# Kernel optimization log

Measured on AMD Instinct MI355X. Metric: run time of the kernel, lower is better.

The kernel has to match this reference:

```python
import jax, jax.numpy as jnp
import numpy as np

BINS = 32
NUM_ACTION = 12


def _conv(x, w, b, stride, pad):
    y = jax.lax.conv_general_dilated(x, w, (stride, stride), [(pad, pad), (pad, pad)],
                                     dimension_numbers=('NCHW', 'OIHW', 'NCHW'))
    return y + b[None, :, None, None]


def _maxpool3s2(x):
    return jax.lax.reduce_window(x, -jnp.inf, jax.lax.max, (1, 1, 3, 3), (1, 1, 2, 2), 'VALID')


def _area_resize(x, oh, ow):
    b, c, h, w = x.shape  # exact area interp when h%oh==0, w%ow==0
    return x.reshape(b, c, oh, h // oh, ow, w // ow).mean(axis=(3, 5))


def _sobel_mag(gray):
    # kornia.filters.Sobel: normalized sobel kernels (abs-sum=1), replicate pad, sqrt(gx^2+gy^2+eps)
    kx = jnp.array([[-1., 0., 1.], [-2., 0., 2.], [-1., 0., 1.]], jnp.float32) / 8.0
    k = jnp.stack([kx, kx.T])[:, None]  # [2,1,3,3]
    p = jnp.pad(gray, ((0, 0), (0, 0), (1, 1), (1, 1)), mode='edge')
    g = jax.lax.conv_general_dilated(p, k, (1, 1), 'VALID',
                                     dimension_numbers=('NCHW', 'OIHW', 'NCHW'))
    return jnp.sqrt(jnp.sum(g * g, axis=1, keepdims=True) + 1e-6)


def _hist_feature(img):
    # Fused replacement for FeatureExtractor's python triple-loop of torch.histc calls.
    # img: [B,1,H,W] with values in [0,1]. Scale 0: whole-image hist; scale 1: the 4
    # quadrants of the full-res image; third bins-slot stays zero (loop only runs 2 scales).
    b, _, h, w = img.shape
    idx = jnp.clip((img[:, 0] * BINS).astype(jnp.int32), 0, BINS - 1)  # [B,H,W]
    hist = lambda i: jnp.zeros((BINS,), jnp.float32).at[i.ravel()].add(1.0)
    h0 = jax.vmap(hist)(idx) / (h * w)                                  # [B,BINS]
    h2, w2 = h // 2, w // 2
    blocks = idx.reshape(b, 2, h2, 2, w2).transpose(0, 1, 3, 2, 4).reshape(b * 4, h2 * w2)
    h1 = jax.vmap(hist)(blocks).reshape(b, 2, 2, BINS) / (h2 * w2)      # [B,2,2,BINS]
    out0 = jnp.broadcast_to(h0[:, :, None, None], (b, BINS, 4, 4))
    out1 = jnp.repeat(jnp.repeat(h1.transpose(0, 3, 1, 2), 2, axis=2), 2, axis=3)
    out2 = jnp.zeros_like(out0)
    return jnp.concatenate([out0, out1, out2], axis=1)                  # [B,3*BINS,4,4]


def _l2norm(x):
    return x / (jnp.linalg.norm(x, axis=1, keepdims=True) + 1e-7)


def _forward(image, w1, b1, w2, b2, w3, b3, w4, b4, w5, b5, fc1_w, fc1_b, fc2_w, fc2_b):
    b = image.shape[0]
    rgb = jnp.stack([image[:, 0], 0.5 * (image[:, 1] + image[:, 2]), image[:, 3]], axis=1)
    # AlexNet conv backbone on area-resized 112x112 -> [B,256,2,2]
    x = _area_resize(rgb, 112, 112)
    x = _maxpool3s2(jax.nn.relu(_conv(x, w1, b1, 4, 2)))
    x = _maxpool3s2(jax.nn.relu(_conv(x, w2, b2, 1, 2)))
    x = jax.nn.relu(_conv(x, w3, b3, 1, 1))
    x = jax.nn.relu(_conv(x, w4, b4, 1, 1))
    x = _maxpool3s2(jax.nn.relu(_conv(x, w5, b5, 1, 1)))
    f_sem = x.reshape(b, -1)                                            # [B,1024]
    gray = (0.299 * rgb[:, 0] + 0.587 * rgb[:, 1] + 0.114 * rgb[:, 2])[:, None]
    f_inten = _hist_feature(gray).reshape(b, -1)                        # [B,1536]
    f_grad = _hist_feature(_sobel_mag(gray)).reshape(b, -1)             # [B,1536]
    f_cat = jnp.concatenate([_l2norm(f_sem), _l2norm(f_inten), _l2norm(f_grad)], axis=1)
    h = jax.nn.relu(f_cat)                                              # Dropout = identity (eval)
    h = jax.nn.relu(h @ fc1_w.T + fc1_b)
    return h @ fc2_w.T + fc2_b                                          # [B,NUM_ACTION]


def setup_inputs() -> dict:
    key = jax.random.key(0)
    ks = jax.random.split(key, 8)
    B = 64
    image = jax.random.uniform(ks[0], (B, 4, 448, 448), jnp.float32)
    w = lambda k, shape, s=0.02: jax.random.normal(k, shape, jnp.float32) * s
    return {
        'image': image,
        'w1': w(ks[1], (64, 3, 11, 11)), 'b1': jnp.zeros((64,), jnp.float32),
        'w2': w(ks[2], (192, 64, 5, 5)), 'b2': jnp.zeros((192,), jnp.float32),
        'w3': w(ks[3], (384, 192, 3, 3)), 'b3': jnp.zeros((384,), jnp.float32),
        'w4': w(ks[4], (256, 384, 3, 3)), 'b4': jnp.zeros((256,), jnp.float32),
        'w5': w(ks[5], (256, 256, 3, 3)), 'b5': jnp.zeros((256,), jnp.float32),
        'fc1_w': w(ks[6], (256, 4096), 0.01), 'fc1_b': jnp.zeros((256,), jnp.float32),
        'fc2_w': w(ks[7], (NUM_ACTION, 256), 0.05), 'fc2_b': jnp.zeros((NUM_ACTION,), jnp.float32),
    }


def reference(image, w1, b1, w2, b2, w3, b3, w4, b4, w5, b5, fc1_w, fc1_b, fc2_w, fc2_b):
    return _forward(image, w1, b1, w2, b2, w3, b3, w4, b4, w5, b5, fc1_w, fc1_b, fc2_w, fc2_b)
```

## Files before the change

### kernel.cpp

```cpp
#include <hip/hip_runtime.h>
#include <math.h>

typedef __attribute__((ext_vector_type(8))) short short8;
typedef __attribute__((ext_vector_type(8))) unsigned short u16x8;
typedef __attribute__((ext_vector_type(4))) float f32x4;
typedef unsigned short ushort_t;

constexpr size_t OFF_HINT = 0;
constexpr size_t OFF_HGRD = OFF_HINT + (size_t)64*160;
constexpr size_t OFF_F    = OFF_HGRD + (size_t)64*160;
constexpr size_t OFF_H1   = OFF_F    + (size_t)64*4096;
constexpr size_t OFF_P5   = OFF_H1   + (size_t)64*256;
constexpr size_t OFF_WHI  = OFF_P5   + (size_t)64*1024;
constexpr size_t W1_OFF = 0;         constexpr int K1T = 363,  K1R = 384;
constexpr size_t W2_OFF = 24576;     constexpr int K2T = 1600, K2R = 1664;
constexpr size_t W3_OFF = 344064;    constexpr int K3T = 1728, K3R = 1792;
constexpr size_t W4_OFF = 1032192;   constexpr int K4T = 3456, K4R = 3456;
constexpr size_t W5_OFF = 1916928;   constexpr int K5T = 2304, K5R = 2304;
constexpr size_t WP_U16 = 2506752;
constexpr size_t OFF_WLO  = OFF_WHI + WP_U16/2;
constexpr size_t OFF_RA   = OFF_WLO + WP_U16/2;
constexpr size_t SZ_RA    = (size_t)2583552/2;
constexpr size_t A4P_U16  = 786432;
constexpr size_t OFF_RB   = OFF_RA + SZ_RA;
constexpr size_t SZ_RB    = (size_t)2985984/2;
constexpr size_t WS_FLOATS = OFF_RB + SZ_RB;

__device__ __forceinline__ void bf16split(float v, unsigned short& hi, unsigned short& lo) {
  union { float f; unsigned u; } a; a.f = v;
  unsigned uh = (a.u + 0x7FFFu + ((a.u >> 16) & 1u)) >> 16;
  hi = (unsigned short)uh;
  union { unsigned u; float f; } b; b.u = uh << 16;
  float rem = v - b.f;
  union { float f; unsigned u; } c; c.f = rem;
  lo = (unsigned short)((c.u + 0x7FFFu + ((c.u >> 16) & 1u)) >> 16);
}
__device__ __forceinline__ ushort_t f2bf(float f) {
  union { float f; unsigned u; } a; a.f = f;
  return (ushort_t)((a.u + 0x7FFFu + ((a.u >> 16) & 1u)) >> 16);
}
__device__ __forceinline__ float bf2f(ushort_t u) {
  union { unsigned u; float f; } a; a.u = ((unsigned)u) << 16; return a.f;
}

__global__ __launch_bounds__(256) void k_wsplit_all(const float* __restrict__ w1,
                                                    const float* __restrict__ w2,
                                                    const float* __restrict__ w3,
                                                    const float* __restrict__ w4,
                                                    const float* __restrict__ w5,
                                                    ushort_t* __restrict__ whi,
                                                    ushort_t* __restrict__ wlo) {
  const size_t idx = (size_t)blockIdx.x * 256 + threadIdx.x;
  if (idx >= WP_U16) return;
  const float* w; int kt, kr; size_t base;
  if (idx < W2_OFF)                { w = w1; kt = K1T; kr = K1R; base = W1_OFF; }
  else if (idx < W3_OFF)           { w = w2; kt = K2T; kr = K2R; base = W2_OFF; }
  else if (idx < W4_OFF)           { w = w3; kt = K3T; kr = K3R; base = W3_OFF; }
  else if (idx < W5_OFF)           { w = w4; kt = K4T; kr = K4R; base = W4_OFF; }
  else                             { w = w5; kt = K5T; kr = K5R; base = W5_OFF; }
  const size_t rel = idx - base;
  const int m = (int)(rel / kr), k = (int)(rel - (size_t)m * kr);
  const float v = (k < kt) ? w[(size_t)m * kt + k] : 0.f;
  unsigned short h, l;
  bf16split(v, h, l);
  whi[idx] = h; wlo[idx] = l;
}

__global__ __launch_bounds__(256) void k_preproc(const float* __restrict__ img,
                                                 float* __restrict__ hint,
                                                 float* __restrict__ hgrd,
                                                 ushort_t* __restrict__ x0) {
  const int b = blockIdx.x, s = blockIdx.y;
  const int r0 = s * 8;
  __shared__ float gs[10][448];
  __shared__ unsigned char lh[64 * 260];
  __shared__ ushort_t part[8 * 112 * 3];
  const int tid = threadIdx.x;
  for (int i = tid; i < (64 * 260) / 4; i += 256) ((unsigned*)lh)[i] = 0u;
  const float* ib = img + (size_t)b * 4 * 200704;
  for (int i = tid; i < 10 * 112; i += 256) {
    const int rr = i / 112, cc = i % 112, c4 = cc * 4;
    int r = r0 + rr - 1; r = r < 0 ? 0 : (r > 447 ? 447 : r);
    const size_t o = (size_t)r * 448 + c4;
    const float4 vr = *(const float4*)&ib[o];
    const float4 g1 = *(const float4*)&ib[200704 + o];
    const float4 g2 = *(const float4*)&ib[2 * 200704 + o];
    const float4 vb = *(const float4*)&ib[3 * 200704 + o];
    float4 g;
    g.x = 0.299f * vr.x + 0.587f * (0.5f * (g1.x + g2.x)) + 0.114f * vb.x;
    g.y = 0.299f * vr.y + 0.587f * (0.5f * (g1.y + g2.y)) + 0.114f * vb.y;
    g.z = 0.299f * vr.z + 0.587f * (0.5f * (g1.z + g2.z)) + 0.114f * vb.z;
    g.w = 0.299f * vr.w + 0.587f * (0.5f * (g1.w + g2.w)) + 0.114f * vb.w;
    *(float4*)&gs[rr][c4] = g;
    if (rr >= 1 && rr <= 8) {
      const float sr = vr.x + vr.y + vr.z + vr.w;
      const float sg = 0.5f * (g1.x + g2.x) + 0.5f * (g1.y + g2.y)
                     + 0.5f * (g1.z + g2.z) + 0.5f * (g1.w + g2.w);
      const float sb = vb.x + vb.y + vb.z + vb.w;
      ushort_t* pp = &part[((rr - 1) * 112 + cc) * 3];
      pp[0] = f2bf(sr); pp[1] = f2bf(sg); pp[2] = f2bf(sb);
    }
  }
  __syncthreads();
  for (int i = tid; i < 672; i += 256) {
    const int cc = i % 112;
    const int t  = i / 112;
    const int or2 = t & 1, ch = t >> 1;
    float sum = 0.f;
    #pragma unroll
    for (int rw = 0; rw < 4; ++rw)
      sum += bf2f(part[((or2 * 4 + rw) * 112 + cc) * 3 + ch]);
    x0[(((size_t)b * 3 + ch) * 116 + 2 + 2 * s + or2) * 116 + 2 + cc] = f2bf(sum * (1.f / 16.f));
  }
  for (int i = tid; i < 8 * 112; i += 256) {
    const int dr = i / 112, c4 = (i % 112) * 4;
    const unsigned colbit = (c4 >= 224) ? 1u : 0u;
    const float4 m1 = *(const float4*)&gs[dr + 1][c4];
    const float gv[4] = {m1.x, m1.y, m1.z, m1.w};
    #pragma unroll
    for (int j = 0; j < 4; ++j) {
      int bin = (int)(gv[j] * 32.f); bin = bin > 31 ? 31 : (bin < 0 ? 0 : bin);
      lh[(colbit * 32u + (unsigned)bin) * 260u + (unsigned)tid]++;
    }
  }
  __syncthreads();
  const unsigned rowbit = (s >= 28) ? 1u : 0u;
  {
    const int key = tid >> 2, quarter = tid & 3;
    const unsigned* row = (const unsigned*)&lh[(unsigned)key * 260u];
    unsigned sum = 0;
    #pragma unroll
    for (int d = 0; d < 16; ++d) {
      const unsigned v = row[quarter * 16 + d];
      sum += (v & 0xFFu) + ((v >> 8) & 0xFFu) + ((v >> 16) & 0xFFu) + (v >> 24);
    }
    sum += __shfl_down(sum, 1, 64);
    sum += __shfl_down(sum, 2, 64);
    if (quarter == 0) {
      const int colbit2 = key >> 5, bin = key & 31;
      atomicAdd(&hint[(size_t)b * 160 + 32 + (rowbit * 2 + colbit2) * 32 + bin], (float)sum);
    }
  }
  __syncthreads();
  for (int i = tid; i < (64 * 260) / 4; i += 256) ((unsigned*)lh)[i] = 0u;
  __syncthreads();
  for (int i = tid; i < 8 * 112; i += 256) {
    const int dr = i / 112, c4 = (i % 112) * 4;
    const unsigned colbit = (c4 >= 224) ? 1u : 0u;
    const int cl = c4 > 0 ? c4 - 1 : 0;
    const int cr = c4 < 444 ? c4 + 4 : 447;
    const float4 m0 = *(const float4*)&gs[dr][c4];
    const float4 m1 = *(const float4*)&gs[dr + 1][c4];
    const float4 m2 = *(const float4*)&gs[dr + 2][c4];
    const float r0v[6] = {gs[dr][cl],     m0.x, m0.y, m0.z, m0.w, gs[dr][cr]};
    const float r1v[6] = {gs[dr + 1][cl], m1.x, m1.y, m1.z, m1.w, gs[dr + 1][cr]};
    const float r2v[6] = {gs[dr + 2][cl], m2.x, m2.y, m2.z, m2.w, gs[dr + 2][cr]};
    #pragma unroll
    for (int j = 0; j < 4; ++j) {
      const float gx = (-r0v[j] + r0v[j + 2] - 2.f * r1v[j] + 2.f * r1v[j + 2]
                        - r2v[j] + r2v[j + 2]) * 0.125f;
      const float gy = (-r0v[j] - 2.f * r0v[j + 1] - r0v[j + 2]
                        + r2v[j] + 2.f * r2v[j + 1] + r2v[j + 2]) * 0.125f;
      const float mag = sqrtf(gx * gx + gy * gy + 1e-6f);
      int sb = (int)(mag * 32.f); sb = sb > 31 ? 31 : (sb < 0 ? 0 : sb);
      lh[(colbit * 32u + (unsigned)sb) * 260u + (unsigned)tid]++;
    }
  }
  __syncthreads();
  {
    const int key = tid >> 2, quarter = tid & 3;
    const unsigned* row = (const unsigned*)&lh[(unsigned)key * 260u];
    unsigned sum = 0;
    #pragma unroll
    for (int d = 0; d < 16; ++d) {
      const unsigned v = row[quarter * 16 + d];
      sum += (v & 0xFFu) + ((v >> 8) & 0xFFu) + ((v >> 16) & 0xFFu) + (v >> 24);
    }
    sum += __shfl_down(sum, 1, 64);
    sum += __shfl_down(sum, 2, 64);
    if (quarter == 0) {
      const int colbit2 = key >> 5, bin = key & 31;
      atomicAdd(&hgrd[(size_t)b * 160 + 32 + (rowbit * 2 + colbit2) * 32 + bin], (float)sum);
    }
  }
}

template<int CIN, int HP, int WP, int KH, int KW, int STRIDE, int OH, int OW,
         int OHP, int OWP, int OPAD, int M, int MT>
__global__ __launch_bounds__(512) void k_conv_mfma(const ushort_t* __restrict__ in,
                                                   const ushort_t* __restrict__ whi_,
                                                   const ushort_t* __restrict__ wlo_,
                                                   const float* __restrict__ bias,
                                                   ushort_t* __restrict__ out) {
  constexpr int K_TOT  = CIN * KH * KW;
  constexpr int K_ROUND = ((K_TOT + 127) / 128) * 128;
  constexpr int GSTEPS = K_ROUND / 128;
  constexpr int KHW = KH * KW;
  constexpr int NPB = OH * OW;
  constexpr int WROWS = MT / 16;
  constexpr int TGRP  = 4 / WROWS;
  constexpr int TFRAG = 4 / TGRP;
  __shared__ ushort_t Bs[2][2][64 * 64];
  __shared__ ushort_t ftab[K_ROUND];
  const int tid = threadIdx.x;
  const int lane = tid & 63, wv = tid >> 6;
  const int g = wv >> 2, wg = wv & 3;
  const int sub = tid & 255;
  const int n0 = blockIdx.x * 64, m0 = blockIdx.y * MT;
  for (int k = tid; k < K_ROUND; k += 512) {
    const int c = k / KHW, kr = k - c * KHW;
    const int ky = kr / KW, kx = kr - (kr / KW) * KW;
    ftab[k] = (k < K_TOT) ? (ushort_t)(2 * ((c * HP + ky) * WP + kx)) : (ushort_t)0;
  }
  const int col = sub & 63, kc2 = sub >> 6;
  const int nb = n0 + col;
  const int bB = nb / NPB, rB = nb % NPB;
  const int oyB = rB / OW, oxB = rB % OW;
  const char* baseB = (const char*)(in + (size_t)bB * CIN * HP * WP)
                      + 2 * (oyB * STRIDE * WP + oxB * STRIDE);
  const int wm = wg % WROWS, tg = wg / WROWS;
  const int mrow = m0 + wm * 16 + (lane & 15);
  const ushort_t* wh = whi_ + (size_t)mrow * K_ROUND;
  const ushort_t* wl = wlo_ + (size_t)mrow * K_ROUND;
  const int kA = (lane >> 4) * 8;
  f32x4 acc[TFRAG] = {};
  const int kb0 = g * GSTEPS * 64;
  __syncthreads();

  u16x8 rb0, rb1;
  short8 rah0, ral0, rah1, ral1;
  {
    const int kb = kb0;
    const u16x8 f0 = *(const u16x8*)&ftab[kb + kc2 * 16];
    const u16x8 f1 = *(const u16x8*)&ftab[kb + kc2 * 16 + 8];
    #pragma unroll
    for (int j = 0; j < 8; ++j) rb0[j] = *(const ushort_t*)(baseB + f0[j]);
    #pragma unroll
    for (int j = 0; j < 8; ++j) rb1[j] = *(const ushort_t*)(baseB + f1[j]);
    rah0 = *(const short8*)&wh[kb + kA];
    ral0 = *(const short8*)&wl[kb + kA];
    rah1 = *(const short8*)&wh[kb + 32 + kA];
    ral1 = *(const short8*)&wl[kb + 32 + kA];
  }
  {
    const int c0 = kc2 * 2, c1 = c0 + 1;
    *(u16x8*)&Bs[g][0][col * 64 + ((c0 ^ (col & 7)) * 8)] = rb0;
    *(u16x8*)&Bs[g][0][col * 64 + ((c1 ^ (col & 7)) * 8)] = rb1;
  }
  __syncthreads();
  int cur = 0;
  for (int step = 0; step < GSTEPS; ++step) {
    const short8 a_h0 = rah0, a_l0 = ral0, a_h1 = rah1, a_l1 = ral1;
    if (step + 1 < GSTEPS) {
      const int kb = kb0 + (step + 1) * 64;
      const u16x8 f0 = *(const u16x8*)&ftab[kb + kc2 * 16];
      const u16x8 f1 = *(const u16x8*)&ftab[kb + kc2 * 16 + 8];
      #pragma unroll
      for (int j = 0; j < 8; ++j) rb0[j] = *(const ushort_t*)(baseB + f0[j]);
      #pragma unroll
      for (int j = 0; j < 8; ++j) rb1[j] = *(const ushort_t*)(baseB + f1[j]);
      rah0 = *(const short8*)&wh[kb + kA];
      ral0 = *(const short8*)&wl[kb + kA];
      rah1 = *(const short8*)&wh[kb + 32 + kA];
      ral1 = *(const short8*)&wl[kb + 32 + kA];
    }
    #pragma unroll
    for (int s = 0; s < 2; ++s) {
      const short8 a_h = s ? a_h1 : a_h0;
      const short8 a_l = s ? a_l1 : a_l0;
      const int cA = s * 4 + (lane >> 4);
      #pragma unroll
      for (int tt = 0; tt < TFRAG; ++tt) {
        const int t = tg * TFRAG + tt;
        const int coln = t * 16 + (lane & 15);
        const short8 b_v = *(const short8*)&Bs[g][cur][coln * 64 + ((cA ^ (coln & 7)) * 8)];
        acc[tt] = __builtin_amdgcn_mfma_f32_16x16x32_bf16(a_h, b_v, acc[tt], 0, 0, 0);
        acc[tt] = __builtin_amdgcn_mfma_f32_16x16x32_bf16(a_l, b_v, acc[tt], 0, 0, 0);
      }
    }
    if (step + 1 < GSTEPS) {
      const int c0 = kc2 * 2, c1 = c0 + 1;
      *(u16x8*)&Bs[g][cur ^ 1][col * 64 + ((c0 ^ (col & 7)) * 8)] = rb0;
      *(u16x8*)&Bs[g][cur ^ 1][col * 64 + ((c1 ^ (col & 7)) * 8)] = rb1;
      __syncthreads();
      cur ^= 1;
    }
  }
  __syncthreads();
  float* scratch = (float*)&Bs[0][0][0];
  if (g == 1) {
    #pragma unroll
    for (int tt = 0; tt < TFRAG; ++tt) {
      const int t = tg * TFRAG + tt;
      #pragma unroll
      for (int q = 0; q < 4; ++q)
        scratch[(wm * 16 + (lane >> 4) * 4 + q) * 64 + t * 16 + (lane & 15)] = acc[tt][q];
    }
  }
  __syncthreads();
  if (g == 0) {
    #pragma unroll
    for (int q = 0; q < 4; ++q) {
      const int m = m0 + wm * 16 + (lane >> 4) * 4 + q;
      const float bi = bias[m];
      #pragma unroll
      for (int tt = 0; tt < TFRAG; ++tt) {
        const int t = tg * TFRAG + tt;
        const int n = n0 + t * 16 + (lane & 15);
        const float v = acc[tt][q]
                      + scratch[(wm * 16 + (lane >> 4) * 4 + q) * 64 + t * 16 + (lane & 15)]
                      + bi;
        const int b = n / NPB, r = n % NPB;
        const int oy = r / OW, ox = r - (r / OW) * OW;
        out[(((size_t)b * M + m) * OHP + OPAD + oy) * OWP + OPAD + ox] = f2bf(fmaxf(v, 0.f));
      }
    }
  }
}

template<int C, int HI, int HO, int HOP, int PAD, bool OUTF32>
__global__ __launch_bounds__(256) void k_pool(const ushort_t* __restrict__ in,
                                              void* __restrict__ out) {
  const int idx = blockIdx.x * 256 + threadIdx.x;
  constexpr int TOT = 64 * C * HOP * HOP;
  if (idx >= TOT) return;
  const int x = idx % HOP;
  const int y = (idx / HOP) % HOP;
  const int c = (idx / (HOP * HOP)) % C;
  const int b = idx / (HOP * HOP * C);
  ushort_t v = 0;
  const int oy = y - PAD, ox = x - PAD;
  if (oy >= 0 && oy < HO && ox >= 0 && ox < HO) {
    const ushort_t* ib = in + (size_t)(b * C + c) * HI * HI + (size_t)(oy * 2) * HI + ox * 2;
    #pragma unroll
    for (int i = 0; i < 3; ++i)
      #pragma unroll
      for (int j = 0; j < 3; ++j) {
        const ushort_t u = ib[i * HI + j];
        v = u > v ? u : v;
      }
  }
  if constexpr (OUTF32) ((float*)out)[idx] = bf2f(v);
  else                  ((ushort_t*)out)[idx] = v;
}

__global__ __launch_bounds__(256) void k_feat(const float* __restrict__ p5,
                                              const float* __restrict__ hint,
                                              const float* __restrict__ hgrad,
                                              float* __restrict__ f) {
  const int b = blockIdx.x, tid = threadIdx.x;
  __shared__ float tmp4[4];
  __shared__ float vals[160];
  const float* ps = p5 + (size_t)b * 1024;
  float* fb = f + (size_t)b * 4096;
  float mv[4]; float ss = 0.f;
  #pragma unroll
  for (int i = 0; i < 4; ++i) { mv[i] = ps[tid + i * 256]; ss += mv[i] * mv[i]; }
  #pragma unroll
  for (int o = 32; o > 0; o >>= 1) ss += __shfl_down(ss, o, 64);
  if ((tid & 63) == 0) tmp4[tid >> 6] = ss;
  __syncthreads();
  const float inv = 1.f / (sqrtf(tmp4[0] + tmp4[1] + tmp4[2] + tmp4[3]) + 1e-7f);
  #pragma unroll
  for (int i = 0; i < 4; ++i) fb[tid + i * 256] = fmaxf(mv[i] * inv, 0.f);
  for (int ft = 0; ft < 2; ++ft) {
    const float* hb = (ft ? hgrad : hint) + (size_t)b * 160;
    __syncthreads();
    if (tid < 160) {
      float cnt;
      if (tid < 32) cnt = hb[32 + tid] + hb[64 + tid] + hb[96 + tid] + hb[128 + tid];
      else          cnt = hb[tid];
      vals[tid] = cnt * (tid < 32 ? (1.f / 200704.f) : (1.f / 50176.f));
    }
    __syncthreads();
    float s2 = 0.f;
    if (tid < 160) s2 = (tid < 32 ? 16.f : 4.f) * vals[tid] * vals[tid];
    #pragma unroll
    for (int o = 32; o > 0; o >>= 1) s2 += __shfl_down(s2, o, 64);
    __syncthreads();
    if ((tid & 63) == 0) tmp4[tid >> 6] = s2;
    __syncthreads();
    const float inv2 = 1.f / (sqrtf(tmp4[0] + tmp4[1] + tmp4[2] + tmp4[3]) + 1e-7f);
    float* fo = fb + 1024 + ft * 1536;
    for (int idx = tid; idx < 1536; idx += 256) {
      const int ch = idx >> 4, i2 = (idx >> 2) & 3, j = idx & 3;
      float v;
      if (ch < 32)      v = vals[ch];
      else if (ch < 64) v = vals[32 + (((i2 >> 1) * 2) + (j >> 1)) * 32 + (ch - 32)];
      else              v = 0.f;
      fo[idx] = fmaxf(v * inv2, 0.f);
    }
  }
}

__global__ __launch_bounds__(256) void k_fc1(const float* __restrict__ f,
                                             const float* __restrict__ w,
                                             const float* __restrict__ bias,
                                             float* __restrict__ h1) {
  const int gid = blockIdx.x * 4 + (threadIdx.x >> 6);
  const int lane = threadIdx.x & 63;
  if (gid >= 64 * 256) return;
  const int oc = gid & 255, b = gid >> 8;
  const float* fb = f + (size_t)b * 4096;
  const float* wr = w + (size_t)oc * 4096;
  float s = 0.f;
  for (int k = lane; k < 4096; k += 64) s += fb[k] * wr[k];
  #pragma unroll
  for (int o = 32; o > 0; o >>= 1) s += __shfl_down(s, o, 64);
  if (lane == 0) h1[(size_t)b * 256 + oc] = fmaxf(s + bias[oc], 0.f);
}

__global__ __launch_bounds__(256) void k_fc2_simple(const float* __restrict__ h1,
                                                    const float* __restrict__ w,
                                                    const float* __restrict__ bias,
                                                    float* __restrict__ out) {
  const int idx = blockIdx.x * 256 + threadIdx.x;
  if (idx >= 64 * 12) return;
  const int oc = idx % 12, b = idx / 12;
  const float* hb = h1 + (size_t)b * 256;
  const float* wr = w + (size_t)oc * 256;
  float s = bias[oc];
  for (int k = 0; k < 256; ++k) s += hb[k] * wr[k];
  out[b * 12 + oc] = s;
}

extern "C" void kernel_launch(void* const* d_in, const int* in_sizes, int n_in,
                              void* d_out, int out_size, void* d_ws, size_t ws_size,
                              hipStream_t stream) {
  const float* img  = (const float*)d_in[0];
  const float* w1 = (const float*)d_in[1];  const float* b1 = (const float*)d_in[2];
  const float* w2 = (const float*)d_in[3];  const float* b2 = (const float*)d_in[4];
  const float* w3 = (const float*)d_in[5];  const float* b3 = (const float*)d_in[6];
  const float* w4 = (const float*)d_in[7];  const float* b4 = (const float*)d_in[8];
  const float* w5 = (const float*)d_in[9];  const float* b5 = (const float*)d_in[10];
  const float* fc1w = (const float*)d_in[11]; const float* fc1b = (const float*)d_in[12];
  const float* fc2w = (const float*)d_in[13]; const float* fc2b = (const float*)d_in[14];
  float* out = (float*)d_out;
  float* ws  = (float*)d_ws;

  float* hint = ws + OFF_HINT;
  float* hgrd = ws + OFF_HGRD;
  float* f    = ws + OFF_F;
  float* h1   = ws + OFF_H1;
  float* p5   = ws + OFF_P5;
  ushort_t* whi = (ushort_t*)(ws + OFF_WHI);
  ushort_t* wlo = (ushort_t*)(ws + OFF_WLO);
  ushort_t* ra  = (ushort_t*)(ws + OFF_RA);
  ushort_t* rb  = (ushort_t*)(ws + OFF_RB);

  hipMemsetAsync(hint, 0, (size_t)2 * 64 * 160 * sizeof(float), stream);
  hipMemsetAsync(ra, 0, (size_t)64 * 3 * 116 * 116 * 2, stream);

  k_wsplit_all<<<(int)((WP_U16 + 255) / 256), 256, 0, stream>>>(w1, w2, w3, w4, w5, whi, wlo);

  k_preproc<<<dim3(64, 56), 256, 0, stream>>>(img, hint, hgrd, ra);

  k_conv_mfma<3,116,116,11,11,4,27,27,27,27,0,64,64>
      <<<dim3(729, 1), 512, 0, stream>>>(ra, whi + W1_OFF, wlo + W1_OFF, b1, rb);
  k_pool<64,27,13,17,2,false><<<(64*64*17*17 + 255)/256, 256, 0, stream>>>(rb, ra);
  k_conv_mfma<64,17,17,5,5,1,13,13,13,13,0,192,64>
      <<<dim3(169, 3), 512, 0, stream>>>(ra, whi + W2_OFF, wlo + W2_OFF, b2, rb);
  k_pool<192,13,6,8,1,false><<<(64*192*8*8 + 255)/256, 256, 0, stream>>>(rb, ra);
  hipMemsetAsync(rb, 0, (size_t)64*384*8*8*2, stream);
  hipMemsetAsync(ra + A4P_U16, 0, (size_t)64*256*8*8*2, stream);
  k_conv_mfma<192,8,8,3,3,1,6,6,8,8,1,384,32>
      <<<dim3(36, 12), 512, 0, stream>>>(ra, whi + W3_OFF, wlo + W3_OFF, b3, rb);
  k_conv_mfma<384,8,8,3,3,1,6,6,8,8,1,256,32>
      <<<dim3(36, 8), 512, 0, stream>>>(rb, whi + W4_OFF, wlo + W4_OFF, b4, ra + A4P_U16);
  k_conv_mfma<256,8,8,3,3,1,6,6,6,6,0,256,32>
      <<<dim3(36, 8), 512, 0, stream>>>(ra + A4P_U16, whi + W5_OFF, wlo + W5_OFF, b5, rb);
  k_pool<256,6,2,2,0,true><<<(64*256*2*2 + 255)/256, 256, 0, stream>>>(rb, p5);

  k_feat<<<64, 256, 0, stream>>>(p5, hint, hgrd, f);
  k_fc1<<<(64*256)/4, 256, 0, stream>>>(f, fc1w, fc1b, h1);
  k_fc2_simple<<<(64*12 + 255)/256, 256, 0, stream>>>(h1, fc2w, fc2b, out);
}
```

Before: 446.7 us.

## Retile conv MFMA warps to 32xN blocks for A/B fragment reuse

Changes each wave's tile in the implicit-GEMM conv kernel from 16 rows by a group of N fragments to 32 rows (two M fragments) by one or two N fragments. Each LDS B fragment now feeds two M fragments and each A fragment feeds NF N fragments, cutting LDS reads per MFMA. Weight fragments are loaded from global memory right before use instead of being prefetched a step ahead in registers. This removes that prefetch latency hiding and assumes MT is 32 or 64.

```diff
diff --git a/kernel.cpp b/kernel.cpp
--- a/kernel.cpp
+++ b/kernel.cpp
@@ -197,9 +197,7 @@
   constexpr int GSTEPS = K_ROUND / 128;
   constexpr int KHW = KH * KW;
   constexpr int NPB = OH * OW;
-  constexpr int WROWS = MT / 16;
-  constexpr int TGRP  = 4 / WROWS;
-  constexpr int TFRAG = 4 / TGRP;
+  constexpr int NF = (MT == 64) ? 2 : 1;
   __shared__ ushort_t Bs[2][2][64 * 64];
   __shared__ ushort_t ftab[K_ROUND];
   const int tid = threadIdx.x;
@@ -218,17 +216,22 @@
   const int oyB = rB / OW, oxB = rB % OW;
   const char* baseB = (const char*)(in + (size_t)bB * CIN * HP * WP)
                       + 2 * (oyB * STRIDE * WP + oxB * STRIDE);
-  const int wm = wg % WROWS, tg = wg / WROWS;
-  const int mrow = m0 + wm * 16 + (lane & 15);
-  const ushort_t* wh = whi_ + (size_t)mrow * K_ROUND;
-  const ushort_t* wl = wlo_ + (size_t)mrow * K_ROUND;
+  const int wm = (MT == 64) ? (wg & 1) : 0;
+  const int wn = (MT == 64) ? (wg >> 1) : wg;
+  const int mbaseL = wm * 32;
+  const int nbaseL = (MT == 64) ? wn * 32 : wn * 16;
+  const int mrow0 = m0 + mbaseL + (lane & 15);
+  const int mrow1 = mrow0 + 16;
+  const ushort_t* wh0 = whi_ + (size_t)mrow0 * K_ROUND;
+  const ushort_t* wl0 = wlo_ + (size_t)mrow0 * K_ROUND;
+  const ushort_t* wh1 = whi_ + (size_t)mrow1 * K_ROUND;
+  const ushort_t* wl1 = wlo_ + (size_t)mrow1 * K_ROUND;
   const int kA = (lane >> 4) * 8;
-  f32x4 acc[TFRAG] = {};
+  f32x4 acc[2][2] = {};
   const int kb0 = g * GSTEPS * 64;
   __syncthreads();
 
   u16x8 rb0, rb1;
-  short8 rah0, ral0, rah1, ral1;
   {
     const int kb = kb0;
     const u16x8 f0 = *(const u16x8*)&ftab[kb + kc2 * 16];
@@ -237,10 +240,6 @@
     for (int j = 0; j < 8; ++j) rb0[j] = *(const ushort_t*)(baseB + f0[j]);
     #pragma unroll
     for (int j = 0; j < 8; ++j) rb1[j] = *(const ushort_t*)(baseB + f1[j]);
-    rah0 = *(const short8*)&wh[kb + kA];
-    ral0 = *(const short8*)&wl[kb + kA];
-    rah1 = *(const short8*)&wh[kb + 32 + kA];
-    ral1 = *(const short8*)&wl[kb + 32 + kA];
   }
   {
     const int c0 = kc2 * 2, c1 = c0 + 1;
@@ -250,32 +249,32 @@
   __syncthreads();
   int cur = 0;
   for (int step = 0; step < GSTEPS; ++step) {
-    const short8 a_h0 = rah0, a_l0 = ral0, a_h1 = rah1, a_l1 = ral1;
+    const int kb = kb0 + step * 64;
     if (step + 1 < GSTEPS) {
-      const int kb = kb0 + (step + 1) * 64;
-      const u16x8 f0 = *(const u16x8*)&ftab[kb + kc2 * 16];
-      const u16x8 f1 = *(const u16x8*)&ftab[kb + kc2 * 16 + 8];
+      const int kbn = kb + 64;
+      const u16x8 f0 = *(const u16x8*)&ftab[kbn + kc2 * 16];
+      const u16x8 f1 = *(const u16x8*)&ftab[kbn + kc2 * 16 + 8];
       #pragma unroll
       for (int j = 0; j < 8; ++j) rb0[j] = *(const ushort_t*)(baseB + f0[j]);
       #pragma unroll
       for (int j = 0; j < 8; ++j) rb1[j] = *(const ushort_t*)(baseB + f1[j]);
-      rah0 = *(const short8*)&wh[kb + kA];
-      ral0 = *(const short8*)&wl[kb + kA];
-      rah1 = *(const short8*)&wh[kb + 32 + kA];
-      ral1 = *(const short8*)&wl[kb + 32 + kA];
     }
     #pragma unroll
     for (int s = 0; s < 2; ++s) {
-      const short8 a_h = s ? a_h1 : a_h0;
-      const short8 a_l = s ? a_l1 : a_l0;
+      const int kk = kb + s * 32 + kA;
+      const short8 ah0 = *(const short8*)&wh0[kk];
+      const short8 al0 = *(const short8*)&wl0[kk];
+      const short8 ah1 = *(const short8*)&wh1[kk];
+      const short8 al1 = *(const short8*)&wl1[kk];
       const int cA = s * 4 + (lane >> 4);
       #pragma unroll
-      for (int tt = 0; tt < TFRAG; ++tt) {
-        const int t = tg * TFRAG + tt;
-        const int coln = t * 16 + (lane & 15);
+      for (int nf = 0; nf < NF; ++nf) {
+        const int coln = nbaseL + nf * 16 + (lane & 15);
         const short8 b_v = *(const short8*)&Bs[g][cur][coln * 64 + ((cA ^ (coln & 7)) * 8)];
-        acc[tt] = __builtin_amdgcn_mfma_f32_16x16x32_bf16(a_h, b_v, acc[tt], 0, 0, 0);
-        acc[tt] = __builtin_amdgcn_mfma_f32_16x16x32_bf16(a_l, b_v, acc[tt], 0, 0, 0);
+        acc[0][nf] = __builtin_amdgcn_mfma_f32_16x16x32_bf16(ah0, b_v, acc[0][nf], 0, 0, 0);
+        acc[0][nf] = __builtin_amdgcn_mfma_f32_16x16x32_bf16(al0, b_v, acc[0][nf], 0, 0, 0);
+        acc[1][nf] = __builtin_amdgcn_mfma_f32_16x16x32_bf16(ah1, b_v, acc[1][nf], 0, 0, 0);
+        acc[1][nf] = __builtin_amdgcn_mfma_f32_16x16x32_bf16(al1, b_v, acc[1][nf], 0, 0, 0);
       }
     }
     if (step + 1 < GSTEPS) {
@@ -290,31 +289,34 @@
   float* scratch = (float*)&Bs[0][0][0];
   if (g == 1) {
     #pragma unroll
-    for (int tt = 0; tt < TFRAG; ++tt) {
-      const int t = tg * TFRAG + tt;
-      #pragma unroll
-      for (int q = 0; q < 4; ++q)
-        scratch[(wm * 16 + (lane >> 4) * 4 + q) * 64 + t * 16 + (lane & 15)] = acc[tt][q];
-    }
+    for (int mf = 0; mf < 2; ++mf)
+      #pragma unroll
+      for (int nf = 0; nf < NF; ++nf)
+        #pragma unroll
+        for (int q = 0; q < 4; ++q)
+          scratch[(mbaseL + mf * 16 + (lane >> 4) * 4 + q) * 64
+                  + nbaseL + nf * 16 + (lane & 15)] = acc[mf][nf][q];
   }
   __syncthreads();
   if (g == 0) {
     #pragma unroll
-    for (int q = 0; q < 4; ++q) {
-      const int m = m0 + wm * 16 + (lane >> 4) * 4 + q;
-      const float bi = bias[m];
-      #pragma unroll
-      for (int tt = 0; tt < TFRAG; ++tt) {
-        const int t = tg * TFRAG + tt;
-        const int n = n0 + t * 16 + (lane & 15);
-        const float v = acc[tt][q]
-                      + scratch[(wm * 16 + (lane >> 4) * 4 + q) * 64 + t * 16 + (lane & 15)]
-                      + bi;
-        const int b = n / NPB, r = n % NPB;
-        const int oy = r / OW, ox = r - (r / OW) * OW;
-        out[(((size_t)b * M + m) * OHP + OPAD + oy) * OWP + OPAD + ox] = f2bf(fmaxf(v, 0.f));
+    for (int mf = 0; mf < 2; ++mf)
+      #pragma unroll
+      for (int q = 0; q < 4; ++q) {
+        const int m = m0 + mbaseL + mf * 16 + (lane >> 4) * 4 + q;
+        const float bi = bias[m];
+        #pragma unroll
+        for (int nf = 0; nf < NF; ++nf) {
+          const int nl = nbaseL + nf * 16 + (lane & 15);
+          const int n = n0 + nl;
+          const float v = acc[mf][nf][q]
+                        + scratch[(mbaseL + mf * 16 + (lane >> 4) * 4 + q) * 64 + nl]
+                        + bi;
+          const int b = n / NPB, r = n % NPB;
+          const int oy = r / OW, ox = r - (r / OW) * OW;
+          out[(((size_t)b * M + m) * OHP + OPAD + oy) * OWP + OPAD + ox] = f2bf(fmaxf(v, 0.f));
+        }
       }
-    }
   }
 }
 
```

Measured after the change: 572.5 us. +28.1%, slower.
